# Performance work log

Hardware: AMD Instinct MI355X
Metric: run time of the kernel (lower is better)

Reference implementation:

```python
import jax, jax.numpy as jnp
import numpy as np

B, T, D, S = 32, 4096, 512, 256
SCALE = 0.1  # time_bias_scale


def setup_inputs() -> dict:
    key = jax.random.key(0)
    ks = jax.random.split(key, 9)
    return {
        "context": jax.random.normal(ks[0], (B, T, D), jnp.float32),
        "t_star": jax.random.uniform(ks[1], (B,), jnp.float32),
        "t_context": jax.random.uniform(ks[2], (B, T, 1), jnp.float32),
        "W1": jax.random.normal(ks[3], (1, D), jnp.float32) / np.sqrt(1.0),
        "b1": jax.random.normal(ks[4], (D,), jnp.float32) * 0.02,
        "W2": jax.random.normal(ks[5], (D, D), jnp.float32) / np.sqrt(D),
        "b2": jax.random.normal(ks[6], (D,), jnp.float32) * 0.02,
        "Wout": jax.random.normal(ks[7], (D, 2 * S), jnp.float32) / np.sqrt(D),
        "bout": jax.random.normal(ks[8], (2 * S,), jnp.float32) * 0.02,
    }


def reference(context, t_star, t_context, W1, b1, W2, b2, Wout, bout):
    # query embed: Linear(1,D) -> SiLU -> Linear(D,D)
    h = jax.nn.silu(t_star[:, None] @ W1 + b1)        # (B, D)
    q = h @ W2 + b2                                   # (B, D)
    # single-query attention scores with additive time bias
    scores = jnp.einsum('bd,btd->bt', q, context)     # (B, T)
    time_bias = -jnp.abs(t_star[:, None] - t_context[..., 0]) / SCALE  # (B, T)
    weights = jax.nn.softmax(scores + time_bias, axis=-1)
    pooled = jnp.einsum('bt,btd->bd', weights, context)  # (B, D)
    out = pooled @ Wout + bout                            # (B, 2S)
    mu, log_sigma = out[:, :S], out[:, S:]
    return (mu, log_sigma)
```

## Files before the change

kernel.cpp:

```cpp
#include <hip/hip_runtime.h>
#include <math.h>

#define BB 32
#define TT 4096
#define DD 512
#define SS 256
#define WPB 96
#define NBLK 768
static constexpr float INV_SCALE = 10.0f;

typedef float f32x4 __attribute__((ext_vector_type(4)));

__global__ __launch_bounds__(512) void k_q(
    const float* __restrict__ t_star, const float* __restrict__ W1,
    const float* __restrict__ b1, const float* __restrict__ W2,
    const float* __restrict__ b2, float* __restrict__ q) {
  const int b   = blockIdx.x >> 3;
  const int jg  = blockIdx.x & 7;
  const int tid = threadIdx.x;
  const int di  = tid & 63;
  const int kg  = tid >> 6;
  __shared__ float h[DD];
  __shared__ float red[8][64];
  {
    float x = t_star[b] * W1[tid] + b1[tid];
    h[tid] = x / (1.0f + __expf(-x));
  }
  __syncthreads();
  const float* w = W2 + jg * 64 + di;
  float acc = 0.0f;
#pragma unroll 8
  for (int kk = 0; kk < 64; ++kk) {
    const int k = kg * 64 + kk;
    acc += h[k] * w[(size_t)k * DD];
  }
  red[kg][di] = acc;
  __syncthreads();
  if (tid < 64) {
    float s = 0.0f;
#pragma unroll
    for (int g = 0; g < 8; ++g) s += red[g][tid];
    q[b * DD + jg * 64 + tid] = s + b2[jg * 64 + tid];
  }
}

#define GLDS(gp, lp)                                                        \
  __builtin_amdgcn_global_load_lds(                                         \
      (const __attribute__((address_space(1))) void*)(gp),                  \
      (__attribute__((address_space(3))) void*)(lp), 16, 0, 2 )

__global__ __launch_bounds__(256) void k_fused(
    const float* __restrict__ ctx, const float* __restrict__ q,
    const float* __restrict__ t_star, const float* __restrict__ t_ctx,
    float* __restrict__ part_pool,
    float* __restrict__ part_ms) {
  __shared__ __align__(16) float lds[4][3][2 * DD];
  const int wid  = threadIdx.x >> 6;
  const int lane = threadIdx.x & 63;
  const int W    = blockIdx.x * 4 + wid;
  const int b    = W / WPB;
  const int v    = W % WPB;
  const int NG   = (v < 32) ? 22 : 21;

  const float4* qp = (const float4*)(q + b * DD);
  const float4 q0 = qp[lane];
  const float4 q1 = qp[64 + lane];
  const float ts = t_star[b];

  const int lg = lane & 31;
  int gidx = lg * WPB + v;
  if (gidx >= TT / 2) gidx = v;
  const float2 tc = *(const float2*)(t_ctx + b * TT + 2 * gidx);
  const float tbx = -fabsf(ts - tc.x) * INV_SCALE;
  const float tby = -fabsf(ts - tc.y) * INV_SCALE;

  float m = -INFINITY, l = 0.0f;
  float4 p0 = {0, 0, 0, 0}, p1 = {0, 0, 0, 0};

  const float* cbatch = ctx + (size_t)b * TT * DD;

#pragma unroll
  for (int g = 0; g < 2; ++g) {
    const float* gb = cbatch + (size_t)(g * WPB + v) * 2 * DD;
    float* sb = &lds[wid][g][0];
#pragma unroll
    for (int piece = 0; piece < 4; ++piece)
      GLDS(gb + piece * 256 + lane * 4, sb + piece * 256);
  }

  int rs = 0, wslot = 2;
  for (int g = 0; g < NG; ++g) {
    if (g + 2 < NG) {
      const float* gb = cbatch + (size_t)((g + 2) * WPB + v) * 2 * DD;
      float* sb = &lds[wid][wslot][0];
#pragma unroll
      for (int piece = 0; piece < 4; ++piece)
        GLDS(gb + piece * 256 + lane * 4, sb + piece * 256);
      asm volatile("s_waitcnt vmcnt(8)" ::: "memory");
    } else if (g + 2 == NG) {
      asm volatile("s_waitcnt vmcnt(4)" ::: "memory");
    } else {
      asm volatile("s_waitcnt vmcnt(0)" ::: "memory");
    }

    const float4* sf = (const float4*)&lds[wid][rs][0];
    const float4 x0 = sf[lane];
    const float4 x1 = sf[64 + lane];
    const float4 y0 = sf[128 + lane];
    const float4 y1 = sf[192 + lane];

    float s0 = x0.x * q0.x + x0.y * q0.y + x0.z * q0.z + x0.w * q0.w +
               x1.x * q1.x + x1.y * q1.y + x1.z * q1.z + x1.w * q1.w;
    float s1 = y0.x * q0.x + y0.y * q0.y + y0.z * q0.z + y0.w * q0.w +
               y1.x * q1.x + y1.y * q1.y + y1.z * q1.z + y1.w * q1.w;
#pragma unroll
    for (int off = 32; off > 0; off >>= 1) {
      s0 += __shfl_xor(s0, off);
      s1 += __shfl_xor(s1, off);
    }
    s0 += __shfl(tbx, g);
    s1 += __shfl(tby, g);

    const float gm = fmaxf(s0, s1);
    const float nm = fmaxf(m, gm);
    const float sc = __expf(m - nm);
    m = nm;
    const float e0 = __expf(s0 - m);
    const float e1 = __expf(s1 - m);
    l = l * sc + e0 + e1;
    p0.x = p0.x * sc + e0 * x0.x + e1 * y0.x;
    p0.y = p0.y * sc + e0 * x0.y + e1 * y0.y;
    p0.z = p0.z * sc + e0 * x0.z + e1 * y0.z;
    p0.w = p0.w * sc + e0 * x0.w + e1 * y0.w;
    p1.x = p1.x * sc + e0 * x1.x + e1 * y1.x;
    p1.y = p1.y * sc + e0 * x1.y + e1 * y1.y;
    p1.z = p1.z * sc + e0 * x1.z + e1 * y1.z;
    p1.w = p1.w * sc + e0 * x1.w + e1 * y1.w;

    rs = (rs == 2) ? 0 : rs + 1;
    wslot = (wslot == 2) ? 0 : wslot + 1;
  }

  f32x4* pp = (f32x4*)(part_pool + (size_t)W * DD);
  f32x4 v0 = {p0.x, p0.y, p0.z, p0.w};
  f32x4 v1 = {p1.x, p1.y, p1.z, p1.w};
  __builtin_nontemporal_store(v0, pp + lane);
  __builtin_nontemporal_store(v1, pp + 64 + lane);
  if (lane == 0) {
    part_ms[W * 2 + 0] = m;
    part_ms[W * 2 + 1] = l;
  }
}

__global__ __launch_bounds__(512) void k_merge(
    const float* __restrict__ part_pool, const float* __restrict__ part_ms,
    float* __restrict__ pool) {
  const int b   = blockIdx.x >> 2;
  const int dg  = blockIdx.x & 3;
  const int tid = threadIdx.x;
  const int lane = tid & 63;
  const int base = b * WPB;
  __shared__ float scl[WPB];
  __shared__ float red[4][128];

  const float mA = part_ms[(base + lane) * 2 + 0];
  const float lA = part_ms[(base + lane) * 2 + 1];
  float mB = -INFINITY, lB = 0.0f;
  if (lane < WPB - 64) {
    mB = part_ms[(base + 64 + lane) * 2 + 0];
    lB = part_ms[(base + 64 + lane) * 2 + 1];
  }
  float M = fmaxf(mA, mB);
#pragma unroll
  for (int off = 32; off > 0; off >>= 1) M = fmaxf(M, __shfl_xor(M, off));
  float Z = __expf(mA - M) * lA + ((lane < WPB - 64) ? __expf(mB - M) * lB : 0.0f);
#pragma unroll
  for (int off = 32; off > 0; off >>= 1) Z += __shfl_xor(Z, off);
  const float invZ = 1.0f / Z;
  if (tid < WPB) scl[tid] = __expf(part_ms[(base + tid) * 2] - M);
  __syncthreads();

  const int dl = tid & 127;
  const int cg = tid >> 7;
  float acc = 0.0f;
#pragma unroll 8
  for (int i = 0; i < 24; ++i) {
    const int c = cg * 24 + i;
    acc += scl[c] * part_pool[((size_t)base + c) * DD + dg * 128 + dl];
  }
  red[cg][dl] = acc;
  __syncthreads();
  if (tid < 128)
    pool[b * DD + dg * 128 + tid] =
        (red[0][tid] + red[1][tid] + red[2][tid] + red[3][tid]) * invZ;
}

__global__ __launch_bounds__(256) void k_out(
    const float* __restrict__ pool, const float* __restrict__ Wout,
    const float* __restrict__ bout, float* __restrict__ out) {
  const int b   = blockIdx.x >> 3;
  const int jg  = blockIdx.x & 7;
  const int tid = threadIdx.x;
  const int kg  = tid >> 6;
  const int j   = tid & 63;
  const int jc  = jg * 64 + j;
  __shared__ float p[DD];
  __shared__ float red[4][64];

  p[tid] = pool[b * DD + tid];
  p[tid + 256] = pool[b * DD + 256 + tid];
  __syncthreads();

  float acc = 0.0f;
#pragma unroll 8
  for (int kk = 0; kk < 128; ++kk) {
    const int k = kg * 128 + kk;
    acc += p[k] * Wout[(size_t)k * DD + jc];
  }
  red[kg][j] = acc;
  __syncthreads();
  if (tid < 64) {
    const int jj = jg * 64 + tid;
    float o = red[0][tid] + red[1][tid] + red[2][tid] + red[3][tid] + bout[jj];
    if (jj < SS) out[b * SS + jj] = o;
    else         out[BB * SS + b * SS + (jj - SS)] = o;
  }
}

extern "C" void kernel_launch(void* const* d_in, const int* in_sizes, int n_in,
                              void* d_out, int out_size, void* d_ws, size_t ws_size,
                              hipStream_t stream) {
  const float* ctx    = (const float*)d_in[0];
  const float* t_star = (const float*)d_in[1];
  const float* t_ctx  = (const float*)d_in[2];
  const float* W1     = (const float*)d_in[3];
  const float* b1     = (const float*)d_in[4];
  const float* W2     = (const float*)d_in[5];
  const float* b2     = (const float*)d_in[6];
  const float* Wout   = (const float*)d_in[7];
  const float* bout   = (const float*)d_in[8];
  float* out = (float*)d_out;

  float* ws = (float*)d_ws;
  float* q         = ws;
  float* part_pool = q + (size_t)BB * DD;
  float* part_ms   = part_pool + (size_t)BB * WPB * DD;
  float* pool      = part_ms + (size_t)BB * WPB * 2;

  k_q<<<BB * 8, 512, 0, stream>>>(t_star, W1, b1, W2, b2, q);
  k_fused<<<NBLK, 256, 0, stream>>>(ctx, q, t_star, t_ctx, part_pool, part_ms);
  k_merge<<<BB * 4, 512, 0, stream>>>(part_pool, part_ms, pool);
  k_out<<<BB * 8, 256, 0, stream>>>(pool, Wout, bout, out);
}
```

Measured before the change: 61.61 us.

## Fuse merge and output projection kernels using per-batch atomic counter barrier

Merges the partial-pool reduction and the output linear layer into one kernel with 8 blocks per batch. Each block reduces a 64-wide slice of the pool, then spins on a per-batch atomic counter (zeroed in k_q) until all 8 slices are written, and finally computes 64 output columns. This removes one kernel launch and its gap. In exchange it relies on all 8 blocks of a batch being co-resident, which a 256-block grid should satisfy, and adds spin-wait and fence overhead.

```diff
diff --git a/kernel.cpp b/kernel.cpp
--- a/kernel.cpp
+++ b/kernel.cpp
@@ -14,12 +14,14 @@
 __global__ __launch_bounds__(512) void k_q(
     const float* __restrict__ t_star, const float* __restrict__ W1,
     const float* __restrict__ b1, const float* __restrict__ W2,
-    const float* __restrict__ b2, float* __restrict__ q) {
+    const float* __restrict__ b2, float* __restrict__ q,
+    int* __restrict__ cnt) {
   const int b   = blockIdx.x >> 3;
   const int jg  = blockIdx.x & 7;
   const int tid = threadIdx.x;
   const int di  = tid & 63;
   const int kg  = tid >> 6;
+  if (tid == 0 && blockIdx.x < BB) cnt[blockIdx.x] = 0;
   __shared__ float h[DD];
   __shared__ float red[8][64];
   {
@@ -152,16 +154,18 @@
   }
 }
 
-__global__ __launch_bounds__(512) void k_merge(
+__global__ __launch_bounds__(512) void k_merge_out(
     const float* __restrict__ part_pool, const float* __restrict__ part_ms,
-    float* __restrict__ pool) {
-  const int b   = blockIdx.x >> 2;
-  const int dg  = blockIdx.x & 3;
+    const float* __restrict__ Wout, const float* __restrict__ bout,
+    float* __restrict__ pool, int* __restrict__ cnt, float* __restrict__ out) {
+  const int b   = blockIdx.x >> 3;
+  const int dg  = blockIdx.x & 7;
   const int tid = threadIdx.x;
   const int lane = tid & 63;
   const int base = b * WPB;
   __shared__ float scl[WPB];
-  __shared__ float red[4][128];
+  __shared__ float red[8][64];
+  __shared__ float pool_s[DD];
 
   const float mA = part_ms[(base + lane) * 2 + 0];
   const float lA = part_ms[(base + lane) * 2 + 1];
@@ -180,48 +184,53 @@
   if (tid < WPB) scl[tid] = __expf(part_ms[(base + tid) * 2] - M);
   __syncthreads();
 
-  const int dl = tid & 127;
-  const int cg = tid >> 7;
+  const int dl = tid & 63;
+  const int cg = tid >> 6;
+  const int d  = dg * 64 + dl;
   float acc = 0.0f;
+#pragma unroll
+  for (int i = 0; i < 12; ++i) {
+    const int c = cg * 12 + i;
+    acc += scl[c] *
+           __builtin_nontemporal_load(&part_pool[((size_t)base + c) * DD + d]);
+  }
+  red[cg][dl] = acc;
+  __syncthreads();
+  if (tid < 64) {
+    float s = 0.0f;
+#pragma unroll
+    for (int g = 0; g < 8; ++g) s += red[g][tid];
+    pool[b * DD + dg * 64 + tid] = s * invZ;
+  }
+  __syncthreads();
+
+  if (tid == 0) {
+    __threadfence();
+    atomicAdd(&cnt[b], 1);
+    while (atomicAdd(&cnt[b], 0) < 8) __builtin_amdgcn_s_sleep(8);
+    __threadfence();
+  }
+  __syncthreads();
+
+  pool_s[tid] = pool[b * DD + tid];
+  if (tid < DD - 512) {}
+  __syncthreads();
+
+  const int j  = dg * 64 + (tid & 63);
+  const int kg = tid >> 6;
+  float a2 = 0.0f;
 #pragma unroll 8
-  for (int i = 0; i < 24; ++i) {
-    const int c = cg * 24 + i;
-    acc += scl[c] * part_pool[((size_t)base + c) * DD + dg * 128 + dl];
-  }
-  red[cg][dl] = acc;
-  __syncthreads();
-  if (tid < 128)
-    pool[b * DD + dg * 128 + tid] =
-        (red[0][tid] + red[1][tid] + red[2][tid] + red[3][tid]) * invZ;
-}
-
-__global__ __launch_bounds__(256) void k_out(
-    const float* __restrict__ pool, const float* __restrict__ Wout,
-    const float* __restrict__ bout, float* __restrict__ out) {
-  const int b   = blockIdx.x >> 3;
-  const int jg  = blockIdx.x & 7;
-  const int tid = threadIdx.x;
-  const int kg  = tid >> 6;
-  const int j   = tid & 63;
-  const int jc  = jg * 64 + j;
-  __shared__ float p[DD];
-  __shared__ float red[4][64];
-
-  p[tid] = pool[b * DD + tid];
-  p[tid + 256] = pool[b * DD + 256 + tid];
-  __syncthreads();
-
-  float acc = 0.0f;
-#pragma unroll 8
-  for (int kk = 0; kk < 128; ++kk) {
-    const int k = kg * 128 + kk;
-    acc += p[k] * Wout[(size_t)k * DD + jc];
-  }
-  red[kg][j] = acc;
+  for (int kk = 0; kk < 64; ++kk) {
+    const int k = kg * 64 + kk;
+    a2 += pool_s[k] * Wout[(size_t)k * DD + j];
+  }
+  red[kg][tid & 63] = a2;
   __syncthreads();
   if (tid < 64) {
-    const int jj = jg * 64 + tid;
-    float o = red[0][tid] + red[1][tid] + red[2][tid] + red[3][tid] + bout[jj];
+    const int jj = dg * 64 + tid;
+    float o = bout[jj];
+#pragma unroll
+    for (int g = 0; g < 8; ++g) o += red[g][tid];
     if (jj < SS) out[b * SS + jj] = o;
     else         out[BB * SS + b * SS + (jj - SS)] = o;
   }
@@ -246,9 +255,10 @@
   float* part_pool = q + (size_t)BB * DD;
   float* part_ms   = part_pool + (size_t)BB * WPB * DD;
   float* pool      = part_ms + (size_t)BB * WPB * 2;
-
-  k_q<<<BB * 8, 512, 0, stream>>>(t_star, W1, b1, W2, b2, q);
+  int*   cnt       = (int*)(pool + (size_t)BB * DD);
+
+  k_q<<<BB * 8, 512, 0, stream>>>(t_star, W1, b1, W2, b2, q, cnt);
   k_fused<<<NBLK, 256, 0, stream>>>(ctx, q, t_star, t_ctx, part_pool, part_ms);
-  k_merge<<<BB * 4, 512, 0, stream>>>(part_pool, part_ms, pool);
-  k_out<<<BB * 8, 256, 0, stream>>>(pool, Wout, bout, out);
-}
+  k_merge_out<<<BB * 8, 512, 0, stream>>>(part_pool, part_ms, Wout, bout,
+                                          pool, cnt, out);
+}
```

Result: slower. 72.33 us (+17.4%).
